# Optimization experiments

Hardware: AMD Instinct MI355X
Metric: run time of the kernel (lower is better)

Reference implementation:

```python
import jax, jax.numpy as jnp
import numpy as np

NUM_HEADS = 16
SPARSITY = 0.1


def setup_inputs() -> dict:
    key = jax.random.key(0)
    ks = jax.random.split(key, 11)
    B, S, D = 2, 2048, 1024
    s = 0.02
    return {
        "query": jax.random.normal(ks[0], (B, S, D), jnp.float32),
        "key": jax.random.normal(ks[1], (B, S, D), jnp.float32),
        "value": jax.random.normal(ks[2], (B, S, D), jnp.float32),
        "Wq": jax.random.normal(ks[3], (D, D), jnp.float32) * s,
        "bq": jax.random.normal(ks[4], (D,), jnp.float32) * s,
        "Wk": jax.random.normal(ks[5], (D, D), jnp.float32) * s,
        "bk": jax.random.normal(ks[6], (D,), jnp.float32) * s,
        "Wv": jax.random.normal(ks[7], (D, D), jnp.float32) * s,
        "bv": jax.random.normal(ks[8], (D,), jnp.float32) * s,
        "Wo": jax.random.normal(ks[9], (D, D), jnp.float32) * s,
        "bo": jax.random.normal(ks[10], (D,), jnp.float32) * s,
    }


def reference(query, key, value, Wq, bq, Wk, bk, Wv, bv, Wo, bo):
    B, Q, D = query.shape
    K = key.shape[1]
    H = NUM_HEADS
    hd = D // H
    scale = 1.0 / np.sqrt(hd).astype(np.float32)

    # projections (torch Linear: x @ W^T + b), split heads -> [B,H,len,hd]
    q = (query @ Wq.T + bq).reshape(B, Q, H, hd).transpose(0, 2, 1, 3)
    k = (key @ Wk.T + bk).reshape(B, K, H, hd).transpose(0, 2, 1, 3)
    v = (value @ Wv.T + bv).reshape(B, K, H, hd).transpose(0, 2, 1, 3)

    # dense relevance scores [B,H,Q,K]
    rel = jnp.einsum('bhqd,bhkd->bhqk', q, k) * scale

    # top-k threshold mask (keep scores >= k-th largest per query row)
    k_per_query = max(1, int(K * SPARSITY))
    top_rel = jax.lax.top_k(rel, k_per_query)[0]
    threshold = top_rel[..., -1:]  # [B,H,Q,1]
    attn = jnp.where(rel < threshold, -jnp.inf, rel)
    attn = jax.nn.softmax(attn, axis=-1)

    out = jnp.einsum('bhqk,bhkd->bhqd', attn, v)
    out = out.transpose(0, 2, 1, 3).reshape(B, Q, D)
    return out @ Wo.T + bo
```

## Files before the change

### kernel.cpp

```cpp
#include <hip/hip_runtime.h>
#include <math.h>

#define D_MODEL 1024
#define SEQ     2048
#define NB      2
#define NH      16
#define HD      64
#define BH      (NB*NH)
#define M_TOK   (NB*SEQ)
#define KSEL    204
#define TQ      16
#define LCAP    256
#define CCAP    96
#define KPW     256

typedef __attribute__((ext_vector_type(8))) short bf16x8;
typedef __attribute__((ext_vector_type(4))) float f32x4;
typedef __attribute__((ext_vector_type(4))) unsigned short us4;
typedef __attribute__((ext_vector_type(8))) unsigned short us8;

__device__ __forceinline__ unsigned short f2bf(float x) {
    unsigned u = __float_as_uint(x);
    return (unsigned short)((u + 0x7FFFu + ((u >> 16) & 1u)) >> 16);
}
__device__ __forceinline__ float bf2f(unsigned short h) {
    return __uint_as_float(((unsigned)h) << 16);
}

__device__ __forceinline__ int binOfE(int e) {
    int b = (e + 4194304) >> 15;
    return b < 0 ? 0 : (b > 255 ? 255 : b);
}

__global__ __launch_bounds__(256) void preconv3_kernel(
    const float* __restrict__ s0, const float* __restrict__ s1,
    const float* __restrict__ s2,
    unsigned short* __restrict__ h0, unsigned short* __restrict__ l0,
    unsigned short* __restrict__ h1, unsigned short* __restrict__ l1,
    unsigned short* __restrict__ h2, unsigned short* __restrict__ l2)
{
    const float* src; unsigned short* hi; unsigned short* lo;
    if (blockIdx.y == 0)      { src = s0; hi = h0; lo = l0; }
    else if (blockIdx.y == 1) { src = s1; hi = h1; lo = l1; }
    else                      { src = s2; hi = h2; lo = l2; }
    int i = (blockIdx.x * 256 + threadIdx.x) * 4;
    float4 v = *(const float4*)(src + i);
    float e[4] = {v.x, v.y, v.z, v.w};
    us4 h, l;
#pragma unroll
    for (int k = 0; k < 4; ++k) {
        unsigned short hh = f2bf(e[k]);
        h[k] = hh; l[k] = f2bf(e[k] - bf2f(hh));
    }
    *(us4*)(hi + i) = h;
    *(us4*)(lo + i) = l;
}

__global__ __launch_bounds__(256) void preconv1_kernel(
    const float* __restrict__ src,
    unsigned short* __restrict__ hi, unsigned short* __restrict__ lo)
{
    int i = (blockIdx.x * 256 + threadIdx.x) * 4;
    float4 v = *(const float4*)(src + i);
    float e[4] = {v.x, v.y, v.z, v.w};
    us4 h, l;
#pragma unroll
    for (int k = 0; k < 4; ++k) {
        unsigned short hh = f2bf(e[k]);
        h[k] = hh; l[k] = f2bf(e[k] - bf2f(hh));
    }
    *(us4*)(hi + i) = h;
    *(us4*)(lo + i) = l;
}

template<int MODE, int TERMS, int AF32>
__device__ __forceinline__ void mfma_gemm_body(
    const float* __restrict__ Xf,
    const unsigned short* __restrict__ XH, const unsigned short* __restrict__ XL,
    const unsigned short* __restrict__ WH, const unsigned short* __restrict__ WL,
    const float* __restrict__ bias,
    float* __restrict__ Cf, unsigned short* __restrict__ Chi,
    unsigned short* __restrict__ Clo, unsigned short* lds)
{
    unsigned short* Ah = lds;
    unsigned short* Al = lds + 4096;
    unsigned short* Bh = lds + 8192;
    unsigned short* Bl = lds + 12288;

    const int tid  = threadIdx.x;
    const int lane = tid & 63;
    const int w    = tid >> 6;
    const int mq   = w & 1;
    const int nq   = w >> 1;
    const int m0   = blockIdx.y * 128;
    const int n0   = blockIdx.x * 128;

    f32x4 acc[4][4];
#pragma unroll
    for (int i = 0; i < 4; ++i)
#pragma unroll
        for (int j = 0; j < 4; ++j) acc[i][j] = (f32x4){0.f, 0.f, 0.f, 0.f};

    for (int k0 = 0; k0 < D_MODEL; k0 += 32) {
        us8 b8h[2], b8l[2], a8h[2], a8l[2];
        float4 xa[4];
#pragma unroll
        for (int r2 = 0; r2 < 2; ++r2) {
            int f = tid + 256 * r2;
            int row = f >> 2, k8 = f & 3;
            size_t g = (size_t)(n0 + row) * D_MODEL + k0 + k8 * 8;
            b8h[r2] = *(const us8*)(WH + g);
            b8l[r2] = *(const us8*)(WL + g);
        }
        if (AF32) {
#pragma unroll
            for (int r = 0; r < 4; ++r) {
                int f = tid + 256 * r;
                int row = f >> 3, q4 = f & 7;
                xa[r] = *(const float4*)(Xf + (size_t)(m0 + row) * D_MODEL + k0 + q4 * 4);
            }
        } else {
#pragma unroll
            for (int r2 = 0; r2 < 2; ++r2) {
                int f = tid + 256 * r2;
                int row = f >> 2, k8 = f & 3;
                size_t g = (size_t)(m0 + row) * D_MODEL + k0 + k8 * 8;
                a8h[r2] = *(const us8*)(XH + g);
                a8l[r2] = *(const us8*)(XL + g);
            }
        }
        __syncthreads();
#pragma unroll
        for (int r2 = 0; r2 < 2; ++r2) {
            int f = tid + 256 * r2;
            int row = f >> 2, k8 = f & 3;
            int off = (row >> 4) * 512 + ((row & 15) + k8 * 16) * 8;
            *(us8*)(Bh + off) = b8h[r2];
            *(us8*)(Bl + off) = b8l[r2];
        }
        if (AF32) {
#pragma unroll
            for (int r = 0; r < 4; ++r) {
                int f = tid + 256 * r;
                int row = f >> 3, q4 = f & 7;
                int off = (row >> 4) * 512 + ((row & 15) + (q4 >> 1) * 16) * 8 + (q4 & 1) * 4;
                float ax[4] = {xa[r].x, xa[r].y, xa[r].z, xa[r].w};
                us4 ahv, alv;
#pragma unroll
                for (int e = 0; e < 4; ++e) {
                    unsigned short h1 = f2bf(ax[e]);
                    ahv[e] = h1; alv[e] = f2bf(ax[e] - bf2f(h1));
                }
                *(us4*)(Ah + off) = ahv;  *(us4*)(Al + off) = alv;
            }
        } else {
#pragma unroll
            for (int r2 = 0; r2 < 2; ++r2) {
                int f = tid + 256 * r2;
                int row = f >> 2, k8 = f & 3;
                int off = (row >> 4) * 512 + ((row & 15) + k8 * 16) * 8;
                *(us8*)(Ah + off) = a8h[r2];
                *(us8*)(Al + off) = a8l[r2];
            }
        }
        __syncthreads();

        bf16x8 fah[4], fal[4], fbh[4], fbl[4];
#pragma unroll
        for (int i = 0; i < 4; ++i) {
            fah[i] = *(const bf16x8*)(Ah + (mq * 4 + i) * 512 + lane * 8);
            fal[i] = *(const bf16x8*)(Al + (mq * 4 + i) * 512 + lane * 8);
            fbh[i] = *(const bf16x8*)(Bh + (nq * 4 + i) * 512 + lane * 8);
            fbl[i] = *(const bf16x8*)(Bl + (nq * 4 + i) * 512 + lane * 8);
        }
#pragma unroll
        for (int i = 0; i < 4; ++i)
#pragma unroll
            for (int j = 0; j < 4; ++j) {
                acc[i][j] = __builtin_amdgcn_mfma_f32_16x16x32_bf16(fah[i], fbh[j], acc[i][j], 0, 0, 0);
                acc[i][j] = __builtin_amdgcn_mfma_f32_16x16x32_bf16(fah[i], fbl[j], acc[i][j], 0, 0, 0);
                acc[i][j] = __builtin_amdgcn_mfma_f32_16x16x32_bf16(fal[i], fbh[j], acc[i][j], 0, 0, 0);
                if (TERMS == 4)
                    acc[i][j] = __builtin_amdgcn_mfma_f32_16x16x32_bf16(fal[i], fbl[j], acc[i][j], 0, 0, 0);
            }
    }

    const int quad = lane >> 4;
    const int rl   = lane & 15;
#pragma unroll
    for (int jt = 0; jt < 4; ++jt) {
        int n = n0 + nq * 64 + jt * 16 + rl;
        float bn = bias[n];
        int h = n >> 6, dd = n & 63;
#pragma unroll
        for (int it = 0; it < 4; ++it) {
#pragma unroll
            for (int r = 0; r < 4; ++r) {
                int m = m0 + mq * 64 + it * 16 + quad * 4 + r;
                float v = acc[it][jt][r] + bn;
                if (MODE == 0) {
                    Cf[(size_t)m * D_MODEL + n] = v;
                } else {
                    int b = m >> 11, s = m & 2047;
                    size_t o = (size_t)(((b << 4) + h) * SEQ + s) * HD + dd;
                    if (MODE == 1) {
                        Cf[o] = v;
                    } else {
                        unsigned short hi = f2bf(v);
                        Chi[o] = hi;
                        Clo[o] = f2bf(v - bf2f(hi));
                    }
                }
            }
        }
    }
}

__global__ __launch_bounds__(256) void proj_qkv_kernel(
    const float* __restrict__ qin, const float* __restrict__ kin, const float* __restrict__ vin,
    const unsigned short* __restrict__ wqh, const unsigned short* __restrict__ wql,
    const unsigned short* __restrict__ wkh, const unsigned short* __restrict__ wkl,
    const unsigned short* __restrict__ wvh, const unsigned short* __restrict__ wvl,
    const float* __restrict__ bq, const float* __restrict__ bk, const float* __restrict__ bv,
    unsigned short* qhi, unsigned short* qlo,
    unsigned short* khi, unsigned short* klo,
    float* vws)
{
    __shared__ unsigned short lds[16384];
    if (blockIdx.z == 0)
        mfma_gemm_body<2, 4, 1>(qin, nullptr, nullptr, wqh, wql, bq,
                                nullptr, qhi, qlo, lds);
    else if (blockIdx.z == 1)
        mfma_gemm_body<2, 4, 1>(kin, nullptr, nullptr, wkh, wkl, bk,
                                nullptr, khi, klo, lds);
    else
        mfma_gemm_body<1, 3, 1>(vin, nullptr, nullptr, wvh, wvl, bv,
                                vws, nullptr, nullptr, lds);
}

__global__ __launch_bounds__(256) void oproj_kernel(
    const unsigned short* __restrict__ AH, const unsigned short* __restrict__ AL,
    const unsigned short* __restrict__ woh, const unsigned short* __restrict__ wol,
    const float* __restrict__ bo, float* __restrict__ out)
{
    __shared__ unsigned short lds[16384];
    mfma_gemm_body<0, 3, 0>(nullptr, AH, AL, woh, wol, bo,
                            out, nullptr, nullptr, lds);
}

__global__ __launch_bounds__(512, 4) void attn_kernel(
    const unsigned short* __restrict__ qhi, const unsigned short* __restrict__ qlo,
    const unsigned short* __restrict__ khi, const unsigned short* __restrict__ klo,
    const float* __restrict__ vws,
    unsigned short* __restrict__ awsHi, unsigned short* __restrict__ awsLo)
{
    __shared__ union __align__(16) UU {
        int hist[TQ][260];
        struct {
            int2  L[TQ][LCAP];
            float cand[TQ][CCAP];
        } p;
    } u;
    __shared__ float thrv[TQ];
    __shared__ int   kneedS[TQ];
    __shared__ int   sbinS[TQ];
    __shared__ int   candCnt[TQ];
    __shared__ int   cnt[TQ];

    const int tid  = threadIdx.x;
    const int lane = tid & 63;
    const int w    = tid >> 6;
    const int quad = lane >> 4;
    const int rl   = lane & 15;
    const int flat = blockIdx.x;
    const int bh   = (flat & 7) * 4 + ((flat >> 3) & 3);
    const int q0   = (flat >> 5) * TQ;
    const size_t hb = (size_t)bh * SEQ * HD;

    {
        int* hp = &u.hist[0][0];
        for (int i = tid; i < TQ * 260; i += 512) hp[i] = 0;
        if (tid < TQ) { candCnt[tid] = 0; cnt[tid] = 0; }
    }

    const size_t qoff = hb + (size_t)(q0 + rl) * HD + quad * 8;
    bf16x8 bqh0 = *(const bf16x8*)(qhi + qoff);
    bf16x8 bql0 = *(const bf16x8*)(qlo + qoff);
    bf16x8 bqh1 = *(const bf16x8*)(qhi + qoff + 32);
    bf16x8 bql1 = *(const bf16x8*)(qlo + qoff + 32);

    const int kbase = w * KPW;
    __syncthreads();

    unsigned scp[48];
#pragma unroll
    for (int t = 0; t < 16; ++t) {
        const size_t koff = hb + (size_t)(kbase + t * 16 + rl) * HD + quad * 8;
        bf16x8 ah0 = *(const bf16x8*)(khi + koff);
        bf16x8 al0 = *(const bf16x8*)(klo + koff);
        bf16x8 ah1 = *(const bf16x8*)(khi + koff + 32);
        bf16x8 al1 = *(const bf16x8*)(klo + koff + 32);
        f32x4 d0 = {0.f, 0.f, 0.f, 0.f};
        f32x4 d1 = {0.f, 0.f, 0.f, 0.f};
        d0 = __builtin_amdgcn_mfma_f32_16x16x32_bf16(ah0, bqh0, d0, 0, 0, 0);
        d1 = __builtin_amdgcn_mfma_f32_16x16x32_bf16(ah1, bqh1, d1, 0, 0, 0);
        d0 = __builtin_amdgcn_mfma_f32_16x16x32_bf16(ah0, bql0, d0, 0, 0, 0);
        d1 = __builtin_amdgcn_mfma_f32_16x16x32_bf16(ah1, bql1, d1, 0, 0, 0);
        d0 = __builtin_amdgcn_mfma_f32_16x16x32_bf16(al0, bqh0, d0, 0, 0, 0);
        d1 = __builtin_amdgcn_mfma_f32_16x16x32_bf16(al1, bqh1, d1, 0, 0, 0);
        f32x4 d = d0 + d1;
        int e[4];
#pragma unroll
        for (int r = 0; r < 4; ++r) {
            e[r] = (int)__builtin_rintf(d[r] * 262144.f);
            atomicAdd(&u.hist[rl][binOfE(e[r])], 1);
        }
        scp[3*t+0] = ((unsigned)e[0] & 0xFFFFFFu) | ((unsigned)e[1] << 24);
        scp[3*t+1] = (((unsigned)e[1] >> 8) & 0xFFFFu) | ((unsigned)e[2] << 16);
        scp[3*t+2] = (((unsigned)e[2] >> 16) & 0xFFu) | ((unsigned)e[3] << 8);
    }
    __syncthreads();

#pragma unroll
    for (int half = 0; half < 2; ++half) {
        int r = w + half * 8;
        int4 hv = *(const int4*)&u.hist[r][4 * lane];
        int h0 = hv.x, h1 = hv.y, h2 = hv.z, h3 = hv.w;
        int s3 = h3, s2 = h2 + s3, s1 = h1 + s2, s0 = h0 + s1;
        int acc = s0;
#pragma unroll
        for (int off = 1; off < 64; off <<= 1) {
            int v = __shfl_down(acc, off);
            acc += (lane + off < 64) ? v : 0;
        }
        int ehi = acc - s0;
        int suf0 = ehi + s0, suf1 = ehi + s1, suf2 = ehi + s2, suf3 = ehi + s3;
        int selbin = -1, newkn = 0;
        if      (suf3 >= KSEL) { selbin = 4*lane + 3; newkn = KSEL - (suf3 - h3); }
        else if (suf2 >= KSEL) { selbin = 4*lane + 2; newkn = KSEL - (suf2 - h2); }
        else if (suf1 >= KSEL) { selbin = 4*lane + 1; newkn = KSEL - (suf1 - h1); }
        else if (suf0 >= KSEL) { selbin = 4*lane + 0; newkn = KSEL - (suf0 - h0); }
        int pack = ((selbin + 1) << 16) | (newkn & 0xFFFF);
#pragma unroll
        for (int off = 32; off; off >>= 1) {
            int o = __shfl_xor(pack, off);
            pack = pack > o ? pack : o;
        }
        if (lane == 0) {
            sbinS[r]  = (pack >> 16) - 1;
            kneedS[r] = pack & 0xFFFF;
        }
    }
    __syncthreads();

    {
        const int sb = sbinS[rl];
#pragma unroll
        for (int t = 0; t < 16; ++t) {
            unsigned p0 = scp[3*t+0], p1 = scp[3*t+1], p2 = scp[3*t+2];
            int e[4];
            e[0] = ((int)(p0 << 8)) >> 8;
            e[1] = ((int)(((p1 << 8) | (p0 >> 24)) << 8)) >> 8;
            e[2] = ((int)(((p2 << 16) | (p1 >> 16)) << 8)) >> 8;
            e[3] = ((int)p2) >> 8;
#pragma unroll
            for (int r = 0; r < 4; ++r) {
                int b = binOfE(e[r]);
                if (b >= sb) {
                    float dv = (float)e[r] * (1.f / 262144.f);
                    int key = kbase + t * 16 + quad * 4 + r;
                    int pos = atomicAdd(&cnt[rl], 1);
                    if (pos < LCAP)
                        u.p.L[rl][pos] = make_int2(key, __float_as_int(dv));
                    if (b == sb) {
                        int cp = atomicAdd(&candCnt[rl], 1);
                        if (cp < CCAP) u.p.cand[rl][cp] = dv;
                    }
                }
            }
        }
    }
    __syncthreads();

#pragma unroll
    for (int half = 0; half < 2; ++half) {
        int r = w + half * 8;
        int n = candCnt[r]; if (n > CCAP) n = CCAP;
        int kn = kneedS[r];
        bool  a0 = lane < n, a1 = lane + 64 < n;
        float x0 = a0 ? u.p.cand[r][lane]      : 0.f;
        float x1 = a1 ? u.p.cand[r][lane + 64] : 0.f;
        int g0 = 0, e0 = 0, g1 = 0, e1 = 0;
        for (int j = 0; j < n; ++j) {
            float c = u.p.cand[r][j];
            g0 += (c > x0);  e0 += (c == x0);
            g1 += (c > x1);  e1 += (c == x1);
        }
        float best = -1e30f;
        if (a0 && g0 < kn && g0 + e0 >= kn) best = x0;
        if (a1 && g1 < kn && g1 + e1 >= kn) best = best > x1 ? best : x1;
#pragma unroll
        for (int off = 32; off; off >>= 1) {
            float o = __shfl_xor(best, off);
            best = best > o ? best : o;
        }
        if (lane == 0) thrv[r] = best;
    }
    __syncthreads();

    {
        const int b = bh >> 4, h = bh & 15;
        const int slot = lane >> 4;
        const int d16  = lane & 15;
        const float* Vp = vws + hb + d16 * 4;

        const int r0 = w, r1 = w + 8;
        int n0 = cnt[r0]; if (n0 > LCAP) n0 = LCAP;
        int n1 = cnt[r1]; if (n1 > LCAP) n1 = LCAP;
        const float t0 = thrv[r0], t1 = thrv[r1];
        const int nmax = n0 > n1 ? n0 : n1;
        f32x4 a0 = {0.f,0.f,0.f,0.f}, a1 = {0.f,0.f,0.f,0.f};
        float z0 = 0.f, z1 = 0.f;

        for (int j = 0; j < nmax; j += 8) {
            int ia = j + slot, ib = j + 4 + slot;
            int i0a = ia < n0 ? ia : 0,  i0b = ib < n0 ? ib : 0;
            int i1a = ia < n1 ? ia : 0,  i1b = ib < n1 ? ib : 0;
            int2 p0a = u.p.L[r0][i0a];
            int2 p0b = u.p.L[r0][i0b];
            int2 p1a = u.p.L[r1][i1a];
            int2 p1b = u.p.L[r1][i1b];
            float s0a = __int_as_float(p0a.y), s0b = __int_as_float(p0b.y);
            float s1a = __int_as_float(p1a.y), s1b = __int_as_float(p1b.y);
            float w0a = ((ia < n0) && (s0a >= t0))
                        ? __builtin_amdgcn_exp2f((s0a - t0) * 0.1803368801f) : 0.f;
            float w0b = ((ib < n0) && (s0b >= t0))
                        ? __builtin_amdgcn_exp2f((s0b - t0) * 0.1803368801f) : 0.f;
            float w1a = ((ia < n1) && (s1a >= t1))
                        ? __builtin_amdgcn_exp2f((s1a - t1) * 0.1803368801f) : 0.f;
            float w1b = ((ib < n1) && (s1b >= t1))
                        ? __builtin_amdgcn_exp2f((s1b - t1) * 0.1803368801f) : 0.f;
            float4 v0a = *(const float4*)(Vp + (size_t)p0a.x * HD);
            float4 v0b = *(const float4*)(Vp + (size_t)p0b.x * HD);
            float4 v1a = *(const float4*)(Vp + (size_t)p1a.x * HD);
            float4 v1b = *(const float4*)(Vp + (size_t)p1b.x * HD);
            a0[0] += w0a * v0a.x + w0b * v0b.x;
            a0[1] += w0a * v0a.y + w0b * v0b.y;
            a0[2] += w0a * v0a.z + w0b * v0b.z;
            a0[3] += w0a * v0a.w + w0b * v0b.w;
            a1[0] += w1a * v1a.x + w1b * v1b.x;
            a1[1] += w1a * v1a.y + w1b * v1b.y;
            a1[2] += w1a * v1a.z + w1b * v1b.z;
            a1[3] += w1a * v1a.w + w1b * v1b.w;
            z0 += w0a + w0b; z1 += w1a + w1b;
        }
#pragma unroll
        for (int off = 16; off < 64; off <<= 1) {
            a0[0] += __shfl_xor(a0[0], off); a0[1] += __shfl_xor(a0[1], off);
            a0[2] += __shfl_xor(a0[2], off); a0[3] += __shfl_xor(a0[3], off);
            a1[0] += __shfl_xor(a1[0], off); a1[1] += __shfl_xor(a1[1], off);
            a1[2] += __shfl_xor(a1[2], off); a1[3] += __shfl_xor(a1[3], off);
            z0 += __shfl_xor(z0, off);       z1 += __shfl_xor(z1, off);
        }
        if (slot == 0) {
            float zr0 = 1.f / z0, zr1 = 1.f / z1;
            float o0[4] = {a0[0]*zr0, a0[1]*zr0, a0[2]*zr0, a0[3]*zr0};
            float o1[4] = {a1[0]*zr1, a1[1]*zr1, a1[2]*zr1, a1[3]*zr1};
            size_t off0 = ((size_t)(b * SEQ) + q0 + r0) * D_MODEL + h * HD + d16 * 4;
            size_t off1 = ((size_t)(b * SEQ) + q0 + r1) * D_MODEL + h * HD + d16 * 4;
            us4 h0, l0, h1, l1;
#pragma unroll
            for (int e = 0; e < 4; ++e) {
                unsigned short hh0 = f2bf(o0[e]);
                h0[e] = hh0; l0[e] = f2bf(o0[e] - bf2f(hh0));
                unsigned short hh1 = f2bf(o1[e]);
                h1[e] = hh1; l1[e] = f2bf(o1[e] - bf2f(hh1));
            }
            *(us4*)(awsHi + off0) = h0;  *(us4*)(awsLo + off0) = l0;
            *(us4*)(awsHi + off1) = h1;  *(us4*)(awsLo + off1) = l1;
        }
    }
}

extern "C" void kernel_launch(void* const* d_in, const int* in_sizes, int n_in,
                              void* d_out, int out_size, void* d_ws, size_t ws_size,
                              hipStream_t stream)
{
    const float* query = (const float*)d_in[0];
    const float* key   = (const float*)d_in[1];
    const float* value = (const float*)d_in[2];
    const float* Wq    = (const float*)d_in[3];
    const float* bq    = (const float*)d_in[4];
    const float* Wk    = (const float*)d_in[5];
    const float* bk    = (const float*)d_in[6];
    const float* Wv    = (const float*)d_in[7];
    const float* bv    = (const float*)d_in[8];
    const float* Wo    = (const float*)d_in[9];
    const float* bo    = (const float*)d_in[10];
    float* out = (float*)d_out;

    char* wsb = (char*)d_ws;
    const size_t MB = 1024u * 1024u;
    unsigned short* qhi = (unsigned short*)(wsb);
    unsigned short* qlo = (unsigned short*)(wsb + 8 * MB);
    unsigned short* khi = (unsigned short*)(wsb + 16 * MB);
    unsigned short* klo = (unsigned short*)(wsb + 24 * MB);
    float* vws          = (float*)(wsb + 32 * MB);
    unsigned short* wqh = (unsigned short*)(wsb + 48 * MB);
    unsigned short* wql = (unsigned short*)(wsb + 50 * MB);
    unsigned short* wkh = (unsigned short*)(wsb + 52 * MB);
    unsigned short* wkl = (unsigned short*)(wsb + 54 * MB);
    unsigned short* wvh = (unsigned short*)(wsb + 56 * MB);
    unsigned short* wvl = (unsigned short*)(wsb + 58 * MB);
    unsigned short* awsHi = (unsigned short*)(wsb + 48 * MB);
    unsigned short* awsLo = (unsigned short*)(wsb + 56 * MB);
    unsigned short* woh = (unsigned short*)(wsb);
    unsigned short* wol = (unsigned short*)(wsb + 2 * MB);

    preconv3_kernel<<<dim3(1024, 3), 256, 0, stream>>>(
        Wq, Wk, Wv, wqh, wql, wkh, wkl, wvh, wvl);

    dim3 g1(D_MODEL / 128, M_TOK / 128, 3);
    proj_qkv_kernel<<<g1, 256, 0, stream>>>(query, key, value,
                                            wqh, wql, wkh, wkl, wvh, wvl,
                                            bq, bk, bv,
                                            qhi, qlo, khi, klo, vws);

    dim3 g2((SEQ / TQ) * BH);
    attn_kernel<<<g2, 512, 0, stream>>>(qhi, qlo, khi, klo, vws, awsHi, awsLo);

    preconv1_kernel<<<1024, 256, 0, stream>>>(Wo, woh, wol);

    dim3 g3(D_MODEL / 128, M_TOK / 128);
    oproj_kernel<<<g3, 256, 0, stream>>>(awsHi, awsLo, woh, wol, bo, out);
}
```

Before: 699.6 us.

## Replace candidate-sort threshold search with two-level sub-histogram radix select

The top-k threshold search used to collect every candidate in the boundary bin (up to 96) and rank them with an O(n^2) compare loop. It now builds a 64-entry sub-histogram for the boundary bin and finds the target sub-bin with a wave prefix scan. Only that sub-bin's values (up to 32) go through the compare loop, and the threshold stays in registers instead of shared memory. The cost is an extra pass over the packed scores and one more barrier. Address math for K and V also switches to 32-bit unsigned offsets from a hoisted base pointer, which removes some 64-bit arithmetic.

```diff
diff --git a/kernel.cpp b/kernel.cpp
--- a/kernel.cpp
+++ b/kernel.cpp
@@ -11,7 +11,7 @@
 #define KSEL    204
 #define TQ      16
 #define LCAP    256
-#define CCAP    96
+#define C2CAP   32
 #define KPW     256
 
 typedef __attribute__((ext_vector_type(8))) short bf16x8;
@@ -30,6 +30,9 @@
 __device__ __forceinline__ int binOfE(int e) {
     int b = (e + 4194304) >> 15;
     return b < 0 ? 0 : (b > 255 ? 255 : b);
+}
+__device__ __forceinline__ int subOfE(int e) {
+    return (e >> 9) & 63;
 }
 
 __global__ __launch_bounds__(256) void preconv3_kernel(
@@ -257,15 +260,19 @@
     __shared__ union __align__(16) UU {
         int hist[TQ][260];
         struct {
-            int2  L[TQ][LCAP];
-            float cand[TQ][CCAP];
+            int2 L[TQ][LCAP];
+            union {
+                int   subh[TQ][64];
+                float cand2[TQ][C2CAP];
+            } s;
         } p;
     } u;
-    __shared__ float thrv[TQ];
-    __shared__ int   kneedS[TQ];
-    __shared__ int   sbinS[TQ];
-    __shared__ int   candCnt[TQ];
-    __shared__ int   cnt[TQ];
+    __shared__ int kneedS[TQ];
+    __shared__ int sbinS[TQ];
+    __shared__ int selsubS[TQ];
+    __shared__ int kneed2S[TQ];
+    __shared__ int cnt[TQ];
+    __shared__ int cnt2[TQ];
 
     const int tid  = threadIdx.x;
     const int lane = tid & 63;
@@ -280,7 +287,9 @@
     {
         int* hp = &u.hist[0][0];
         for (int i = tid; i < TQ * 260; i += 512) hp[i] = 0;
-        if (tid < TQ) { candCnt[tid] = 0; cnt[tid] = 0; }
+        int* sp = &u.p.s.subh[0][0];
+        for (int i = tid; i < TQ * 64; i += 512) sp[i] = 0;
+        if (tid < TQ) { cnt[tid] = 0; cnt2[tid] = 0; }
     }
 
     const size_t qoff = hb + (size_t)(q0 + rl) * HD + quad * 8;
@@ -289,17 +298,20 @@
     bf16x8 bqh1 = *(const bf16x8*)(qhi + qoff + 32);
     bf16x8 bql1 = *(const bf16x8*)(qlo + qoff + 32);
 
+    const unsigned short* Kh = khi + hb;
+    const unsigned short* Kl = klo + hb;
+
     const int kbase = w * KPW;
     __syncthreads();
 
     unsigned scp[48];
 #pragma unroll
     for (int t = 0; t < 16; ++t) {
-        const size_t koff = hb + (size_t)(kbase + t * 16 + rl) * HD + quad * 8;
-        bf16x8 ah0 = *(const bf16x8*)(khi + koff);
-        bf16x8 al0 = *(const bf16x8*)(klo + koff);
-        bf16x8 ah1 = *(const bf16x8*)(khi + koff + 32);
-        bf16x8 al1 = *(const bf16x8*)(klo + koff + 32);
+        const unsigned ko = (unsigned)(kbase + t * 16 + rl) * HD + quad * 8;
+        bf16x8 ah0 = *(const bf16x8*)(Kh + ko);
+        bf16x8 al0 = *(const bf16x8*)(Kl + ko);
+        bf16x8 ah1 = *(const bf16x8*)(Kh + ko + 32);
+        bf16x8 al1 = *(const bf16x8*)(Kl + ko + 32);
         f32x4 d0 = {0.f, 0.f, 0.f, 0.f};
         f32x4 d1 = {0.f, 0.f, 0.f, 0.f};
         d0 = __builtin_amdgcn_mfma_f32_16x16x32_bf16(ah0, bqh0, d0, 0, 0, 0);
@@ -372,10 +384,8 @@
                     int pos = atomicAdd(&cnt[rl], 1);
                     if (pos < LCAP)
                         u.p.L[rl][pos] = make_int2(key, __float_as_int(dv));
-                    if (b == sb) {
-                        int cp = atomicAdd(&candCnt[rl], 1);
-                        if (cp < CCAP) u.p.cand[rl][cp] = dv;
-                    }
+                    if (b == sb)
+                        atomicAdd(&u.p.s.subh[rl][subOfE(e[r])], 1);
                 }
             }
         }
@@ -385,39 +395,86 @@
 #pragma unroll
     for (int half = 0; half < 2; ++half) {
         int r = w + half * 8;
-        int n = candCnt[r]; if (n > CCAP) n = CCAP;
-        int kn = kneedS[r];
-        bool  a0 = lane < n, a1 = lane + 64 < n;
-        float x0 = a0 ? u.p.cand[r][lane]      : 0.f;
-        float x1 = a1 ? u.p.cand[r][lane + 64] : 0.f;
-        int g0 = 0, e0 = 0, g1 = 0, e1 = 0;
+        int kneed = kneedS[r];
+        int h = u.p.s.subh[r][lane];
+        int acc = h;
+#pragma unroll
+        for (int off = 1; off < 64; off <<= 1) {
+            int v = __shfl_down(acc, off);
+            acc += (lane + off < 64) ? v : 0;
+        }
+        int sel = -1, kn2 = 0;
+        if (acc >= kneed) { sel = lane; kn2 = kneed - (acc - h); }
+        int pack = ((sel + 1) << 16) | (kn2 & 0xFFFF);
+#pragma unroll
+        for (int off = 32; off; off >>= 1) {
+            int o = __shfl_xor(pack, off);
+            pack = pack > o ? pack : o;
+        }
+        if (lane == 0) {
+            selsubS[r] = (pack >> 16) - 1;
+            kneed2S[r] = pack & 0xFFFF;
+        }
+    }
+    __syncthreads();
+
+    {
+        const int sb = sbinS[rl];
+        const int ss = selsubS[rl];
+#pragma unroll
+        for (int t = 0; t < 16; ++t) {
+            unsigned p0 = scp[3*t+0], p1 = scp[3*t+1], p2 = scp[3*t+2];
+            int e[4];
+            e[0] = ((int)(p0 << 8)) >> 8;
+            e[1] = ((int)(((p1 << 8) | (p0 >> 24)) << 8)) >> 8;
+            e[2] = ((int)(((p2 << 16) | (p1 >> 16)) << 8)) >> 8;
+            e[3] = ((int)p2) >> 8;
+#pragma unroll
+            for (int r = 0; r < 4; ++r) {
+                if (binOfE(e[r]) == sb && subOfE(e[r]) == ss) {
+                    int cp = atomicAdd(&cnt2[rl], 1);
+                    if (cp < C2CAP)
+                        u.p.s.cand2[rl][cp] = (float)e[r] * (1.f / 262144.f);
+                }
+            }
+        }
+    }
+    __syncthreads();
+
+    float bestA = -1e30f, bestB = -1e30f;
+#pragma unroll
+    for (int half = 0; half < 2; ++half) {
+        int r = w + half * 8;
+        int n = cnt2[r]; if (n > C2CAP) n = C2CAP;
+        int kn = kneed2S[r];
+        bool  a0 = lane < n;
+        float x0 = a0 ? u.p.s.cand2[r][lane] : 0.f;
+        int g0 = 0, e0 = 0;
         for (int j = 0; j < n; ++j) {
-            float c = u.p.cand[r][j];
+            float c = u.p.s.cand2[r][j];
             g0 += (c > x0);  e0 += (c == x0);
-            g1 += (c > x1);  e1 += (c == x1);
         }
         float best = -1e30f;
         if (a0 && g0 < kn && g0 + e0 >= kn) best = x0;
-        if (a1 && g1 < kn && g1 + e1 >= kn) best = best > x1 ? best : x1;
 #pragma unroll
         for (int off = 32; off; off >>= 1) {
             float o = __shfl_xor(best, off);
             best = best > o ? best : o;
         }
-        if (lane == 0) thrv[r] = best;
-    }
-    __syncthreads();
+        if (half == 0) bestA = best; else bestB = best;
+    }
 
     {
         const int b = bh >> 4, h = bh & 15;
         const int slot = lane >> 4;
         const int d16  = lane & 15;
-        const float* Vp = vws + hb + d16 * 4;
+        const float* Vb = vws + hb;
+        const unsigned dof = d16 * 4;
 
         const int r0 = w, r1 = w + 8;
         int n0 = cnt[r0]; if (n0 > LCAP) n0 = LCAP;
         int n1 = cnt[r1]; if (n1 > LCAP) n1 = LCAP;
-        const float t0 = thrv[r0], t1 = thrv[r1];
+        const float t0 = bestA, t1 = bestB;
         const int nmax = n0 > n1 ? n0 : n1;
         f32x4 a0 = {0.f,0.f,0.f,0.f}, a1 = {0.f,0.f,0.f,0.f};
         float z0 = 0.f, z1 = 0.f;
@@ -440,10 +497,10 @@
                         ? __builtin_amdgcn_exp2f((s1a - t1) * 0.1803368801f) : 0.f;
             float w1b = ((ib < n1) && (s1b >= t1))
                         ? __builtin_amdgcn_exp2f((s1b - t1) * 0.1803368801f) : 0.f;
-            float4 v0a = *(const float4*)(Vp + (size_t)p0a.x * HD);
-            float4 v0b = *(const float4*)(Vp + (size_t)p0b.x * HD);
-            float4 v1a = *(const float4*)(Vp + (size_t)p1a.x * HD);
-            float4 v1b = *(const float4*)(Vp + (size_t)p1b.x * HD);
+            float4 v0a = *(const float4*)(Vb + ((unsigned)p0a.x * HD + dof));
+            float4 v0b = *(const float4*)(Vb + ((unsigned)p0b.x * HD + dof));
+            float4 v1a = *(const float4*)(Vb + ((unsigned)p1a.x * HD + dof));
+            float4 v1b = *(const float4*)(Vb + ((unsigned)p1b.x * HD + dof));
             a0[0] += w0a * v0a.x + w0b * v0b.x;
             a0[1] += w0a * v0a.y + w0b * v0b.y;
             a0[2] += w0a * v0a.z + w0b * v0b.z;
```

Result: slower. 775.3 us (+10.8%).
